# Optimization experiments

Measured on AMD Instinct MI355X. Metric: run time of the kernel, lower is better.

## Reference

```python
import jax, jax.numpy as jnp
import numpy as np

B, L, HIDDEN = 64, 200, 256
HEADS = 8
MAX_WIDTH = 5
EPS = 1e-5  # F.layer_norm default eps


def _ln(x):
    # F.layer_norm with no learned affine
    m = jnp.mean(x, axis=-1, keepdims=True)
    v = jnp.mean((x - m) ** 2, axis=-1, keepdims=True)
    return (x - m) * jax.lax.rsqrt(v + EPS)


def _area_pool(x, max_width, mode):
    # x: [B, H, L, D] -> pooled spans of widths 1..max_width (valid windows),
    # concatenated along the memory axis: M = sum_w (L - w + 1)
    Lx = x.shape[2]
    outs = []
    for w in range(1, max_width + 1):
        # [w, B, H, L-w+1, D] stack of shifted slices (w <= 5, tiny loop)
        win = jnp.stack([x[:, :, i:Lx - w + 1 + i, :] for i in range(w)], axis=0)
        if mode == 'max':
            outs.append(win.max(axis=0))
        elif mode == 'mean':
            outs.append(win.mean(axis=0))
        else:  # 'sum'
            outs.append(win.sum(axis=0))
    return jnp.concatenate(outs, axis=2)


def _mha_area(q_in, k_in, v_in, Wq, bq, Wk, bk, Wv, bv, Wo, bo):
    # per-head size equals hidden_size (key_query_size_hidden = hidden_size)
    Bq, Lq, _ = q_in.shape
    Dh = Wq.shape[1] // HEADS

    def split(x):
        return x.reshape(x.shape[0], x.shape[1], HEADS, Dh).transpose(0, 2, 1, 3)

    q = split(q_in @ Wq + bq)  # [B, H, Lq, Dh]
    k = split(k_in @ Wk + bk)
    v = split(v_in @ Wv + bv)
    k_area = _area_pool(k, MAX_WIDTH, 'max')   # aggr='max' key pooling
    v_area = _area_pool(v, MAX_WIDTH, 'sum')   # values pooled by sum (t2t default)
    scale = jnp.asarray(1.0 / np.sqrt(Dh), q.dtype)
    logits = jnp.einsum('bhqd,bhmd->bhqm', q, k_area) * scale
    attn = jax.nn.softmax(logits, axis=-1)  # dropout inactive at eval
    out = jnp.einsum('bhqm,bhmd->bhqd', attn, v_area)
    out = out.transpose(0, 2, 1, 3).reshape(Bq, Lq, HEADS * Dh)
    return out @ Wo + bo


def setup_inputs() -> dict:
    key = jax.random.key(0)
    ks = jax.random.split(key, 16)
    stdv = 1.0 / np.sqrt(HIDDEN)
    u = lambda k, shp: jax.random.uniform(k, shp, jnp.float32, -stdv, stdv)
    HD = HEADS * HIDDEN  # 2048
    return {
        'A': jax.random.normal(ks[0], (B, L, L), jnp.float32),
        'hidden': jax.random.normal(ks[1], (B, L, HIDDEN), jnp.float32),
        'Wq': u(ks[2], (HIDDEN, HD)), 'bq': u(ks[3], (HD,)),
        'Wk': u(ks[4], (HIDDEN, HD)), 'bk': u(ks[5], (HD,)),
        'Wv': u(ks[6], (HIDDEN, HD)), 'bv': u(ks[7], (HD,)),
        'Wo': u(ks[8], (HD, HIDDEN)), 'bo': u(ks[9], (HIDDEN,)),
        'W1': u(ks[10], (HIDDEN, 4 * HIDDEN)), 'b1': u(ks[11], (4 * HIDDEN,)),
        'W2': u(ks[12], (4 * HIDDEN, HIDDEN)), 'b2': u(ks[13], (HIDDEN,)),
    }


def reference(A, hidden, Wq, bq, Wk, bk, Wv, bv, Wo, bo, W1, b1, W2, b2):
    # step = 1 -> single ATTNCell; A is unused by ATTNCell (matches source)
    attn1 = _mha_area(hidden, hidden, hidden, Wq, bq, Wk, bk, Wv, bv, Wo, bo)
    attn1 = _ln(attn1 + hidden)
    attn2 = _mha_area(attn1, hidden, hidden, Wq, bq, Wk, bk, Wv, bv, Wo, bo)
    attn2 = _ln(attn1 + attn2)  # F.dropout inactive (eval)
    x = jax.nn.relu(attn2 @ W1 + b1) @ W2 + b2
    return _ln(attn2 + x)
```

## Files before the change

kernel.cpp:

```cpp
#include <hip/hip_runtime.h>
#include <hip/hip_bf16.h>
#include <cstdint>
#include <cstddef>

#define BATCH 64
#define LSEQ 200
#define HID 256
#define NH 8
#define DH 256
#define HD (NH*DH)
#define MROWS (BATCH*LSEQ)
#define EPS 1e-5f
#define CSCALE 0.09014195f

typedef unsigned short ushort_t;
typedef __attribute__((ext_vector_type(8))) short bf16x8;
typedef __attribute__((ext_vector_type(8))) unsigned short u16x8;
typedef __attribute__((ext_vector_type(4))) float f32x4;

__device__ __forceinline__ float b2f(ushort_t u) {
    union { unsigned int i; float f; } c; c.i = ((unsigned int)u) << 16; return c.f;
}
__device__ __forceinline__ ushort_t f2b(float f) {
    __hip_bfloat16 h = __float2bfloat16(f);
    union { __hip_bfloat16 h; ushort_t u; } c; c.h = h; return c.u;
}
__device__ __forceinline__ float to_f32(float x) { return x; }
__device__ __forceinline__ float to_f32(ushort_t x) { return b2f(x); }
__device__ __forceinline__ void store_val(float* p, float v) { *p = v; }
__device__ __forceinline__ void store_val(ushort_t* p, float v) { *p = f2b(v); }

__device__ __forceinline__ u16x8 bmax8(u16x8 a, u16x8 b) {
    union U { u16x8 v; __hip_bfloat162 h[4]; };
    U ua, ub, r; ua.v = a; ub.v = b;
    #pragma unroll
    for (int i = 0; i < 4; ++i) r.h[i] = __hmax2(ua.h[i], ub.h[i]);
    return r.v;
}
__device__ __forceinline__ u16x8 badd8(u16x8 a, u16x8 b) {
    union U { u16x8 v; __hip_bfloat162 h[4]; };
    U ua, ub, r; ua.v = a; ub.v = b;
    #pragma unroll
    for (int i = 0; i < 4; ++i) r.h[i] = __hadd2(ua.h[i], ub.h[i]);
    return r.v;
}

__device__ __forceinline__ void gll16(const void* g, void* l) {
    __builtin_amdgcn_global_load_lds(
        (const __attribute__((address_space(1))) unsigned int*)g,
        (__attribute__((address_space(3))) unsigned int*)l, 16, 0, 0);
}

template<bool RELU, int OMODE, bool SCALEC>
__global__ __launch_bounds__(256) void gemm_bt(
    const ushort_t* __restrict__ A, const ushort_t* __restrict__ Bt,
    const float* __restrict__ bias, ushort_t* __restrict__ C,
    int M, int N, int K)
{
    __shared__ ushort_t As[128 * 32];
    __shared__ ushort_t Bs[128 * 32];
    const int t = threadIdx.x;
    const int m0 = blockIdx.y * 128, n0 = blockIdx.x * 128;
    const int wave = t >> 6, lane = t & 63;
    const int l15 = lane & 15, lq = lane >> 4;
    const int wr = wave >> 1, wc = wave & 1;

    f32x4 acc[4][4];
    #pragma unroll
    for (int i = 0; i < 4; ++i)
        #pragma unroll
        for (int j = 0; j < 4; ++j) acc[i][j] = (f32x4){0.f, 0.f, 0.f, 0.f};

    for (int k0 = 0; k0 < K; k0 += 32) {
        __syncthreads();
        #pragma unroll
        for (int i = 0; i < 2; ++i) {
            int li = i * 256 + t;
            int ml = li >> 2, cp = li & 3;
            int cg = cp ^ ((ml ^ (ml >> 2)) & 3);
            gll16(A + (size_t)(m0 + ml) * K + k0 + cg * 8, &As[li * 8]);
        }
        #pragma unroll
        for (int i = 0; i < 2; ++i) {
            int li = i * 256 + t;
            int nl = li >> 2, cp = li & 3;
            int cg = cp ^ ((nl ^ (nl >> 2)) & 3);
            gll16(Bt + (size_t)(n0 + nl) * K + k0 + cg * 8, &Bs[li * 8]);
        }
        __syncthreads();
        bf16x8 af[4], bfr[4];
        #pragma unroll
        for (int i = 0; i < 4; ++i) {
            int r = wr * 64 + i * 16 + l15;
            int pc = lq ^ ((r ^ (r >> 2)) & 3);
            af[i] = *(const bf16x8*)&As[r * 32 + pc * 8];
        }
        #pragma unroll
        for (int j = 0; j < 4; ++j) {
            int r = wc * 64 + j * 16 + l15;
            int pc = lq ^ ((r ^ (r >> 2)) & 3);
            bfr[j] = *(const bf16x8*)&Bs[r * 32 + pc * 8];
        }
        #pragma unroll
        for (int i = 0; i < 4; ++i)
            #pragma unroll
            for (int j = 0; j < 4; ++j)
                acc[i][j] = __builtin_amdgcn_mfma_f32_16x16x32_bf16(af[i], bfr[j], acc[i][j], 0, 0, 0);
    }
    if (OMODE == 2) {
        #pragma unroll
        for (int i = 0; i < 4; ++i) {
            int mbase = m0 + wr * 64 + i * 16 + 4 * lq;
            int bb = (int)(((unsigned)mbase * 5243u) >> 20);
            int ll = mbase - bb * 200;
            #pragma unroll
            for (int j = 0; j < 4; ++j) {
                int n = n0 + wc * 64 + j * 16 + l15;
                float bsv = bias[n];
                ushort4 o4;
                o4.x = f2b(acc[i][j][0] + bsv); o4.y = f2b(acc[i][j][1] + bsv);
                o4.z = f2b(acc[i][j][2] + bsv); o4.w = f2b(acc[i][j][3] + bsv);
                size_t addr = ((size_t)(bb * NH + (n >> 8)) * 256 + (n & 255)) * LSEQ + ll;
                *(ushort4*)&C[addr] = o4;
            }
        }
    } else {
        #pragma unroll
        for (int i = 0; i < 4; ++i) {
            #pragma unroll
            for (int e = 0; e < 4; ++e) {
                int m = m0 + wr * 64 + i * 16 + 4 * lq + e;
                #pragma unroll
                for (int j = 0; j < 4; ++j) {
                    int n = n0 + wc * 64 + j * 16 + l15;
                    float v = acc[i][j][e] + bias[n];
                    if (RELU) v = fmaxf(v, 0.f);
                    if (SCALEC) v *= CSCALE;
                    if (OMODE == 1) {
                        int bb = (int)(((unsigned)m * 5243u) >> 20);
                        int ll = m - bb * 200;
                        size_t addr = ((((size_t)(bb * NH + (n >> 8))) * LSEQ + ll) << 8) + (n & 255);
                        C[addr] = f2b(v);
                    } else {
                        C[(size_t)m * N + n] = f2b(v);
                    }
                }
            }
        }
    }
}

__global__ __launch_bounds__(512, 2) void attn_mfma13(
    const ushort_t* __restrict__ Q, const ushort_t* __restrict__ Khm,
    const ushort_t* __restrict__ Vt, ushort_t* __restrict__ O)
{
    const int id = blockIdx.x;
    const int xcd = id & 7, slot_ = id >> 3;
    const int qt = slot_ & 1;
    const int bh = ((slot_ >> 1) << 3) + xcd;
    const int b = bh >> 3, h = bh & 7;
    const int q0 = qt * 128;
    const int t = threadIdx.x;
    const int wave = t >> 6, lane = t & 63;
    const int l15 = lane & 15, lq = lane >> 4;

    __shared__ ushort_t Ks[64 * 256];
    __shared__ ushort_t Vs[256 * 64];

    const ushort_t* kbh = Khm + (size_t)bh * LSEQ * DH;
    const ushort_t* vtb = Vt + (size_t)bh * DH * LSEQ;
    const ushort_t* qbh = Q + ((size_t)b * LSEQ) * HD + h * DH;
    const int qrow = q0 + wave * 16 + l15;

    bf16x8 qf[8];
    if (qrow < LSEQ) {
        const ushort_t* qp = qbh + (size_t)qrow * HD + 8 * lq;
        #pragma unroll
        for (int g = 0; g < 8; ++g) qf[g] = *(const bf16x8*)(qp + 32 * g);
    } else {
        bf16x8 zf = {0,0,0,0,0,0,0,0};
        #pragma unroll
        for (int g = 0; g < 8; ++g) qf[g] = zf;
    }

    f32x4 oacc[16];
    #pragma unroll
    for (int i = 0; i < 16; ++i) oacc[i] = (f32x4){0.f, 0.f, 0.f, 0.f};
    float l_part = 0.f;

    const int dc = t & 31, mb = t >> 5;
    const int vd = t >> 1, vh = t & 1;

    auto step = [&](bool tail) {
        f32x4 sacc[4];
        __builtin_amdgcn_s_setprio(1);
        #pragma unroll
        for (int ms = 0; ms < 4; ++ms) {
            f32x4 s = (f32x4){0.f, 0.f, 0.f, 0.f};
            const int row = ms * 16 + l15;
            #pragma unroll
            for (int g = 0; g < 8; ++g) {
                const int phys = (lq + 4 * g) ^ l15;
                s = __builtin_amdgcn_mfma_f32_16x16x32_bf16(
                        *(const bf16x8*)&Ks[row * 256 + phys * 8], qf[g], s, 0, 0, 0);
            }
            sacc[ms] = s;
        }
        __builtin_amdgcn_s_setprio(0);
        unsigned int w[8];
        #pragma unroll
        for (int ms = 0; ms < 4; ++ms) {
            float pj[4];
            #pragma unroll
            for (int e = 0; e < 4; ++e) {
                float sv = sacc[ms][e];
                if (tail) {
                    const int slot = ms * 16 + 4 * lq + e;
                    if (((slot & 7) > 7 - (slot >> 3)) || ((slot >> 3) > 4)) sv = -1e30f;
                }
                float p = __builtin_exp2f(sv);
                l_part += p;
                pj[e] = p;
            }
            asm("v_cvt_pk_bf16_f32 %0, %1, %2" : "=v"(w[2*ms])   : "v"(pj[0]), "v"(pj[1]));
            asm("v_cvt_pk_bf16_f32 %0, %1, %2" : "=v"(w[2*ms+1]) : "v"(pj[2]), "v"(pj[3]));
        }
        union FR { unsigned int u[4]; bf16x8 v; };
        FR f0, f1;
        f0.u[0] = w[0]; f0.u[1] = w[1]; f0.u[2] = w[2]; f0.u[3] = w[3];
        f1.u[0] = w[4]; f1.u[1] = w[5]; f1.u[2] = w[6]; f1.u[3] = w[7];
        const bf16x8 pf0 = f0.v, pf1 = f1.v;
        __builtin_amdgcn_s_setprio(1);
        #pragma unroll
        for (int dt = 0; dt < 16; ++dt) {
            const int d = dt * 16 + l15;
            const int p0 = lq ^ (d & 7);
            const int p1 = (lq + 4) ^ (d & 7);
            oacc[dt] = __builtin_amdgcn_mfma_f32_16x16x32_bf16(
                           pf0, *(const bf16x8*)&Vs[d * 64 + p0 * 8], oacc[dt], 0, 0, 0);
            oacc[dt] = __builtin_amdgcn_mfma_f32_16x16x32_bf16(
                           pf1, *(const bf16x8*)&Vs[d * 64 + p1 * 8], oacc[dt], 0, 0, 0);
        }
        __builtin_amdgcn_s_setprio(0);
    };

    for (int ti = 0; ti < 3; ++ti) {
        const int st0 = ti * 64;
        #pragma unroll
        for (int cls = 0; cls < 5; ++cls) {
            u16x8 kf[4];
            #pragma unroll
            for (int k4 = 0; k4 < 4; ++k4)
                kf[k4] = *(const u16x8*)(kbh + (size_t)(st0 + mb + 16 * k4 + cls) * DH + dc * 8);
            __syncthreads();

            #pragma unroll
            for (int k4 = 0; k4 < 4; ++k4) {
                int m = mb + 16 * k4;
                ushort_t* kp = &Ks[m * 256 + ((dc ^ (m & 15)) * 8)];
                *(u16x8*)kp = (cls == 0) ? kf[k4] : bmax8(*(const u16x8*)kp, kf[k4]);
            }
            {
                const ushort_t* vrow = vtb + (size_t)vd * LSEQ + st0 + vh * 32;
                u16x8 va = *(const u16x8*)vrow;
                #pragma unroll
                for (int cl = 0; cl < 4; ++cl) {
                    u16x8 vb = *(const u16x8*)(vrow + (cl + 1) * 8);
                    const int cg = vh * 4 + cl;
                    const int kc = (cg >> 2) * 4 + (cg & 1) * 2;
                    const int par4 = ((cg >> 1) & 1) * 4;
                    ushort_t* plo = &Vs[vd * 64 + ((kc ^ (vd & 7)) * 8) + par4];
                    ushort_t* phi = &Vs[vd * 64 + (((kc + 1) ^ (vd & 7)) * 8) + par4];
                    union VH { u16x8 v; ushort4 h[2]; };
                    VH nv;
                    if (cls == 0) {
                        nv.v = va;
                    } else {
                        u16x8 sh;
                        #pragma unroll
                        for (int j = 0; j < 8; ++j)
                            sh[j] = (j + cls < 8) ? va[j + cls] : vb[j + cls - 8];
                        VH cur;
                        cur.h[0] = *(const ushort4*)plo;
                        cur.h[1] = *(const ushort4*)phi;
                        nv.v = badd8(cur.v, sh);
                    }
                    *(ushort4*)plo = nv.h[0];
                    *(ushort4*)phi = nv.h[1];
                    va = vb;
                }
            }
            __syncthreads();
            step(false);
        }
    }

    {
        __syncthreads();
        if (mb < 8) {
            u16x8 krun = *(const u16x8*)(kbh + (size_t)(192 + mb) * DH + dc * 8);
            const u16x8 kz = {0,0,0,0,0,0,0,0};
            #pragma unroll
            for (int k8 = 0; k8 < 8; ++k8) {
                const bool v = (k8 <= 4) && (mb <= 7 - k8);
                if (k8 > 0 && v)
                    krun = bmax8(krun, *(const u16x8*)(kbh + (size_t)(192 + mb + k8) * DH + dc * 8));
                int slot = k8 * 8 + mb;
                *(u16x8*)&Ks[slot * 256 + ((dc ^ (slot & 15)) * 8)] = v ? krun : kz;
            }
        }
        {
            u16x8 v0 = *(const u16x8*)(vtb + (size_t)vd * LSEQ + 192);
            float f[8];
            #pragma unroll
            for (int e = 0; e < 8; ++e) f[e] = b2f(v0[e]);
            #pragma unroll
            for (int cl = 0; cl < 4; ++cl) {
                const int c = vh * 4 + cl;
                union VH { u16x8 v; ushort4 h[2]; } ov;
                #pragma unroll
                for (int j = 0; j < 8; ++j) ov.v[j] = 0;
                if (c <= 4) {
                    #pragma unroll
                    for (int j = 0; j < 8; ++j) {
                        if (j <= 7 - c) {
                            float acc = 0.f;
                            #pragma unroll
                            for (int u = 0; u <= 4; ++u)
                                if (u <= c) acc += f[j + u];
                            ov.v[j] = f2b(acc);
                        }
                    }
                }
                const int kc = (c >> 2) * 4 + (c & 1) * 2;
                const int par4 = ((c >> 1) & 1) * 4;
                *(ushort4*)&Vs[vd * 64 + ((kc ^ (vd & 7)) * 8) + par4] = ov.h[0];
                *(ushort4*)&Vs[vd * 64 + (((kc + 1) ^ (vd & 7)) * 8) + par4] = ov.h[1];
            }
        }
        __syncthreads();
        step(true);
    }

    l_part += __shfl_xor(l_part, 16);
    l_part += __shfl_xor(l_part, 32);
    const float inv = 1.f / l_part;

    ushort_t* ob = O + ((size_t)b * LSEQ) * HD + h * DH;
    #pragma unroll
    for (int e = 0; e < 4; ++e) {
        const int q = q0 + wave * 16 + 4 * lq + e;
        const float linv = __shfl(inv, 4 * lq + e);
        if (q < LSEQ) {
            #pragma unroll
            for (int dt = 0; dt < 16; ++dt)
                ob[(size_t)q * HD + dt * 16 + l15] = f2b(oacc[dt][e] * linv);
        }
    }
}

template<typename TR, typename TO>
__global__ __launch_bounds__(256) void residual_ln(
    const ushort_t* __restrict__ X, const TR* __restrict__ R, TO* __restrict__ Out)
{
    const int row = blockIdx.x;
    const int t = threadIdx.x;
    const size_t base = (size_t)row * HID;
    float v = b2f(X[base + t]) + to_f32(R[base + t]);
    float s = v, q = v * v;
    #pragma unroll
    for (int o = 32; o > 0; o >>= 1) {
        s += __shfl_xor(s, o, 64);
        q += __shfl_xor(q, o, 64);
    }
    __shared__ float ss[4], sq[4];
    const int wave = t >> 6, lane = t & 63;
    if (lane == 0) { ss[wave] = s; sq[wave] = q; }
    __syncthreads();
    s = ss[0] + ss[1] + ss[2] + ss[3];
    q = sq[0] + sq[1] + sq[2] + sq[3];
    float mean = s * (1.f / HID);
    float var  = q * (1.f / HID) - mean * mean;
    store_val(&Out[base + t], (v - mean) * rsqrtf(var + EPS));
}

__global__ __launch_bounds__(256) void cvt_f32_bf16(const float* __restrict__ in,
                                                    ushort_t* __restrict__ out) {
    const int i = (blockIdx.x * 256 + threadIdx.x) * 4;
    float4 v = *(const float4*)(in + i);
    ushort4 o;
    o.x = f2b(v.x); o.y = f2b(v.y); o.z = f2b(v.z); o.w = f2b(v.w);
    *(ushort4*)(out + i) = o;
}

__global__ __launch_bounds__(256) void wtrans(const float* __restrict__ W,
                                              ushort_t* __restrict__ Wt, int K, int N) {
    __shared__ float tile[32][33];
    const int t = threadIdx.x;
    const int tx = t & 31, ty = t >> 5;
    const int n0 = blockIdx.x * 32, k0 = blockIdx.y * 32;
    #pragma unroll
    for (int s = 0; s < 4; ++s)
        tile[ty + 8 * s][tx] = W[(size_t)(k0 + ty + 8 * s) * N + n0 + tx];
    __syncthreads();
    #pragma unroll
    for (int s = 0; s < 4; ++s)
        Wt[(size_t)(n0 + ty + 8 * s) * K + k0 + tx] = f2b(tile[tx][ty + 8 * s]);
}

extern "C" void kernel_launch(void* const* d_in, const int* in_sizes, int n_in,
                              void* d_out, int out_size, void* d_ws, size_t ws_size,
                              hipStream_t stream) {
    const float* hidden = (const float*)d_in[1];
    const float* Wq = (const float*)d_in[2];  const float* bq = (const float*)d_in[3];
    const float* Wk = (const float*)d_in[4];  const float* bk = (const float*)d_in[5];
    const float* Wv = (const float*)d_in[6];  const float* bv = (const float*)d_in[7];
    const float* Wo = (const float*)d_in[8];  const float* bo = (const float*)d_in[9];
    const float* W1 = (const float*)d_in[10]; const float* b1 = (const float*)d_in[11];
    const float* W2 = (const float*)d_in[12]; const float* b2 = (const float*)d_in[13];
    float* out = (float*)d_out;

    constexpr size_t SZ_BF   = (size_t)MROWS * HD * 2;
    constexpr size_t SZ_HBF  = (size_t)MROWS * HID * 2;
    constexpr size_t SZ_WQKV = (size_t)HID * HD * 2;
    constexpr size_t SZ_W12  = (size_t)HID * 4 * HID * 2;
    char* ws = (char*)d_ws;
    size_t off = 0;
    ushort_t* kb   = (ushort_t*)(ws + off); off += SZ_BF;
    ushort_t* vt   = (ushort_t*)(ws + off); off += SZ_BF;
    ushort_t* qo   = (ushort_t*)(ws + off); off += SZ_BF;
    ushort_t* hb   = (ushort_t*)(ws + off); off += SZ_HBF;
    ushort_t* at1  = (ushort_t*)(ws + off); off += SZ_HBF;
    ushort_t* at2  = (ushort_t*)(ws + off); off += SZ_HBF;
    ushort_t* proj = (ushort_t*)(ws + off); off += SZ_HBF;
    ushort_t* WtQ  = (ushort_t*)(ws + off); off += SZ_WQKV;
    ushort_t* WtK  = (ushort_t*)(ws + off); off += SZ_WQKV;
    ushort_t* WtV  = (ushort_t*)(ws + off); off += SZ_WQKV;
    ushort_t* WtO  = (ushort_t*)(ws + off); off += SZ_WQKV;
    ushort_t* Wt1  = (ushort_t*)(ws + off); off += SZ_W12;
    ushort_t* Wt2  = (ushort_t*)(ws + off); off += SZ_W12;
    if (ws_size < off) return;
    ushort_t* ffn1 = qo;

    dim3 blk(256);
    cvt_f32_bf16<<<MROWS * HID / 1024, blk, 0, stream>>>(hidden, hb);
    wtrans<<<dim3(HD / 32, HID / 32), blk, 0, stream>>>(Wq, WtQ, HID, HD);
    wtrans<<<dim3(HD / 32, HID / 32), blk, 0, stream>>>(Wk, WtK, HID, HD);
    wtrans<<<dim3(HD / 32, HID / 32), blk, 0, stream>>>(Wv, WtV, HID, HD);
    wtrans<<<dim3(HID / 32, HD / 32), blk, 0, stream>>>(Wo, WtO, HD, HID);
    wtrans<<<dim3(4 * HID / 32, HID / 32), blk, 0, stream>>>(W1, Wt1, HID, 4 * HID);
    wtrans<<<dim3(HID / 32, 4 * HID / 32), blk, 0, stream>>>(W2, Wt2, 4 * HID, HID);

    const dim3 gProj(HD / 128, MROWS / 128);
    const dim3 gOut(HID / 128, MROWS / 128);
    const dim3 gF1(4 * HID / 128, MROWS / 128);

    gemm_bt<false, 1, false><<<gProj, blk, 0, stream>>>(hb, WtK, bk, kb, MROWS, HD, HID);
    gemm_bt<false, 2, false><<<gProj, blk, 0, stream>>>(hb, WtV, bv, vt, MROWS, HD, HID);

    gemm_bt<false, 0, true><<<gProj, blk, 0, stream>>>(hb, WtQ, bq, qo, MROWS, HD, HID);
    attn_mfma13<<<2 * BATCH * NH, 512, 0, stream>>>(qo, kb, vt, qo);
    gemm_bt<false, 0, false><<<gOut, blk, 0, stream>>>(qo, WtO, bo, proj, MROWS, HID, HD);
    residual_ln<float, ushort_t><<<MROWS, blk, 0, stream>>>(proj, hidden, at1);

    gemm_bt<false, 0, true><<<gProj, blk, 0, stream>>>(at1, WtQ, bq, qo, MROWS, HD, HID);
    attn_mfma13<<<2 * BATCH * NH, 512, 0, stream>>>(qo, kb, vt, qo);
    gemm_bt<false, 0, false><<<gOut, blk, 0, stream>>>(qo, WtO, bo, proj, MROWS, HID, HD);
    residual_ln<ushort_t, ushort_t><<<MROWS, blk, 0, stream>>>(proj, at1, at2);

    gemm_bt<true, 0, false><<<gF1, blk, 0, stream>>>(at2, Wt1, b1, ffn1, MROWS, 4 * HID, HID);
    gemm_bt<false, 0, false><<<gOut, blk, 0, stream>>>(ffn1, Wt2, b2, proj, MROWS, HID, 4 * HID);
    residual_ln<ushort_t, float><<<MROWS, blk, 0, stream>>>(proj, at2, out);
}
```

Baseline: 977.7 us.

## Halve attention block threads, each wave computing two query tiles sharing K/V LDS reads

The attention kernel now runs 256 threads per block instead of 512. Each wave handles two 16-row query tiles (rows r and r+64), so every K and V fragment read from LDS feeds two MFMAs. The K/V pooling loaders are reworked so the 256 threads cover the same 64-slot tile. This cuts LDS read traffic per MFMA and halves the threads doing the pooling work, at the cost of roughly doubled accumulator registers per thread, which may lower occupancy or cause spills.

```diff
diff --git a/kernel.cpp b/kernel.cpp
--- a/kernel.cpp
+++ b/kernel.cpp
@@ -150,7 +150,7 @@
     }
 }
 
-__global__ __launch_bounds__(512, 2) void attn_mfma13(
+__global__ __launch_bounds__(256, 2) void attn_mfma15(
     const ushort_t* __restrict__ Q, const ushort_t* __restrict__ Khm,
     const ushort_t* __restrict__ Vt, ushort_t* __restrict__ O)
 {
@@ -170,76 +170,94 @@
     const ushort_t* kbh = Khm + (size_t)bh * LSEQ * DH;
     const ushort_t* vtb = Vt + (size_t)bh * DH * LSEQ;
     const ushort_t* qbh = Q + ((size_t)b * LSEQ) * HD + h * DH;
-    const int qrow = q0 + wave * 16 + l15;
-
-    bf16x8 qf[8];
-    if (qrow < LSEQ) {
-        const ushort_t* qp = qbh + (size_t)qrow * HD + 8 * lq;
-        #pragma unroll
-        for (int g = 0; g < 8; ++g) qf[g] = *(const bf16x8*)(qp + 32 * g);
+
+    const int qrA = q0 + wave * 16 + l15;
+    const int qrB = qrA + 64;
+    bf16x8 qfA[8], qfB[8];
+    {
+        const ushort_t* qp = qbh + (size_t)qrA * HD + 8 * lq;
+        #pragma unroll
+        for (int g = 0; g < 8; ++g) qfA[g] = *(const bf16x8*)(qp + 32 * g);
+    }
+    if (qrB < LSEQ) {
+        const ushort_t* qp = qbh + (size_t)qrB * HD + 8 * lq;
+        #pragma unroll
+        for (int g = 0; g < 8; ++g) qfB[g] = *(const bf16x8*)(qp + 32 * g);
     } else {
         bf16x8 zf = {0,0,0,0,0,0,0,0};
         #pragma unroll
-        for (int g = 0; g < 8; ++g) qf[g] = zf;
-    }
-
-    f32x4 oacc[16];
-    #pragma unroll
-    for (int i = 0; i < 16; ++i) oacc[i] = (f32x4){0.f, 0.f, 0.f, 0.f};
-    float l_part = 0.f;
+        for (int g = 0; g < 8; ++g) qfB[g] = zf;
+    }
+
+    f32x4 oaccA[16], oaccB[16];
+    #pragma unroll
+    for (int i = 0; i < 16; ++i) {
+        oaccA[i] = (f32x4){0.f, 0.f, 0.f, 0.f};
+        oaccB[i] = (f32x4){0.f, 0.f, 0.f, 0.f};
+    }
+    float lA = 0.f, lB = 0.f;
 
     const int dc = t & 31, mb = t >> 5;
-    const int vd = t >> 1, vh = t & 1;
+    const int vd = t;
 
     auto step = [&](bool tail) {
-        f32x4 sacc[4];
+        f32x4 sA[4], sB[4];
         __builtin_amdgcn_s_setprio(1);
         #pragma unroll
         for (int ms = 0; ms < 4; ++ms) {
-            f32x4 s = (f32x4){0.f, 0.f, 0.f, 0.f};
+            f32x4 xa = (f32x4){0.f, 0.f, 0.f, 0.f};
+            f32x4 xb = (f32x4){0.f, 0.f, 0.f, 0.f};
             const int row = ms * 16 + l15;
             #pragma unroll
             for (int g = 0; g < 8; ++g) {
                 const int phys = (lq + 4 * g) ^ l15;
-                s = __builtin_amdgcn_mfma_f32_16x16x32_bf16(
-                        *(const bf16x8*)&Ks[row * 256 + phys * 8], qf[g], s, 0, 0, 0);
-            }
-            sacc[ms] = s;
+                const bf16x8 kk = *(const bf16x8*)&Ks[row * 256 + phys * 8];
+                xa = __builtin_amdgcn_mfma_f32_16x16x32_bf16(kk, qfA[g], xa, 0, 0, 0);
+                xb = __builtin_amdgcn_mfma_f32_16x16x32_bf16(kk, qfB[g], xb, 0, 0, 0);
+            }
+            sA[ms] = xa; sB[ms] = xb;
         }
         __builtin_amdgcn_s_setprio(0);
-        unsigned int w[8];
+        unsigned int wA[8], wB[8];
         #pragma unroll
         for (int ms = 0; ms < 4; ++ms) {
-            float pj[4];
+            float pa[4], pb[4];
             #pragma unroll
             for (int e = 0; e < 4; ++e) {
-                float sv = sacc[ms][e];
+                float va_ = sA[ms][e], vb_ = sB[ms][e];
                 if (tail) {
                     const int slot = ms * 16 + 4 * lq + e;
-                    if (((slot & 7) > 7 - (slot >> 3)) || ((slot >> 3) > 4)) sv = -1e30f;
+                    if (((slot & 7) > 7 - (slot >> 3)) || ((slot >> 3) > 4)) {
+                        va_ = -1e30f; vb_ = -1e30f;
+                    }
                 }
-                float p = __builtin_exp2f(sv);
-                l_part += p;
-                pj[e] = p;
-            }
-            asm("v_cvt_pk_bf16_f32 %0, %1, %2" : "=v"(w[2*ms])   : "v"(pj[0]), "v"(pj[1]));
-            asm("v_cvt_pk_bf16_f32 %0, %1, %2" : "=v"(w[2*ms+1]) : "v"(pj[2]), "v"(pj[3]));
+                float ea = __builtin_exp2f(va_);
+                float eb = __builtin_exp2f(vb_);
+                lA += ea; lB += eb;
+                pa[e] = ea; pb[e] = eb;
+            }
+            asm("v_cvt_pk_bf16_f32 %0, %1, %2" : "=v"(wA[2*ms])   : "v"(pa[0]), "v"(pa[1]));
+            asm("v_cvt_pk_bf16_f32 %0, %1, %2" : "=v"(wA[2*ms+1]) : "v"(pa[2]), "v"(pa[3]));
+            asm("v_cvt_pk_bf16_f32 %0, %1, %2" : "=v"(wB[2*ms])   : "v"(pb[0]), "v"(pb[1]));
+            asm("v_cvt_pk_bf16_f32 %0, %1, %2" : "=v"(wB[2*ms+1]) : "v"(pb[2]), "v"(pb[3]));
         }
         union FR { unsigned int u[4]; bf16x8 v; };
-        FR f0, f1;
-        f0.u[0] = w[0]; f0.u[1] = w[1]; f0.u[2] = w[2]; f0.u[3] = w[3];
-        f1.u[0] = w[4]; f1.u[1] = w[5]; f1.u[2] = w[6]; f1.u[3] = w[7];
-        const bf16x8 pf0 = f0.v, pf1 = f1.v;
+        FR a0, a1, b0, b1;
+        a0.u[0] = wA[0]; a0.u[1] = wA[1]; a0.u[2] = wA[2]; a0.u[3] = wA[3];
+        a1.u[0] = wA[4]; a1.u[1] = wA[5]; a1.u[2] = wA[6]; a1.u[3] = wA[7];
+        b0.u[0] = wB[0]; b0.u[1] = wB[1]; b0.u[2] = wB[2]; b0.u[3] = wB[3];
+        b1.u[0] = wB[4]; b1.u[1] = wB[5]; b1.u[2] = wB[6]; b1.u[3] = wB[7];
+        const bf16x8 pfA0 = a0.v, pfA1 = a1.v, pfB0 = b0.v, pfB1 = b1.v;
         __builtin_amdgcn_s_setprio(1);
         #pragma unroll
         for (int dt = 0; dt < 16; ++dt) {
             const int d = dt * 16 + l15;
-            const int p0 = lq ^ (d & 7);
-            const int p1 = (lq + 4) ^ (d & 7);
-            oacc[dt] = __builtin_amdgcn_mfma_f32_16x16x32_bf16(
-                           pf0, *(const bf16x8*)&Vs[d * 64 + p0 * 8], oacc[dt], 0, 0, 0);
-            oacc[dt] = __builtin_amdgcn_mfma_f32_16x16x32_bf16(
-                           pf1, *(const bf16x8*)&Vs[d * 64 + p1 * 8], oacc[dt], 0, 0, 0);
+            const bf16x8 v0 = *(const bf16x8*)&Vs[d * 64 + ((lq ^ (d & 7)) * 8)];
+            const bf16x8 v1 = *(const bf16x8*)&Vs[d * 64 + (((lq + 4) ^ (d & 7)) * 8)];
+            oaccA[dt] = __builtin_amdgcn_mfma_f32_16x16x32_bf16(pfA0, v0, oaccA[dt], 0, 0, 0);
+            oaccA[dt] = __builtin_amdgcn_mfma_f32_16x16x32_bf16(pfA1, v1, oaccA[dt], 0, 0, 0);
+            oaccB[dt] = __builtin_amdgcn_mfma_f32_16x16x32_bf16(pfB0, v0, oaccB[dt], 0, 0, 0);
+            oaccB[dt] = __builtin_amdgcn_mfma_f32_16x16x32_bf16(pfB1, v1, oaccB[dt], 0, 0, 0);
         }
         __builtin_amdgcn_s_setprio(0);
     };
@@ -250,23 +268,29 @@
         for (int cls = 0; cls < 5; ++cls) {
             u16x8 kf[4];
             #pragma unroll
-            for (int k4 = 0; k4 < 4; ++k4)
-                kf[k4] = *(const u16x8*)(kbh + (size_t)(st0 + mb + 16 * k4 + cls) * DH + dc * 8);
+            for (int k8 = 0; k8 < 4; ++k8)
+                kf[k8] = *(const u16x8*)(kbh + (size_t)(st0 + mb + 8 * k8 + cls) * DH + dc * 8);
             __syncthreads();
 
             #pragma unroll
-            for (int k4 = 0; k4 < 4; ++k4) {
-                int m = mb + 16 * k4;
+            for (int k8 = 0; k8 < 4; ++k8) {
+                int m = mb + 8 * k8;
                 ushort_t* kp = &Ks[m * 256 + ((dc ^ (m & 15)) * 8)];
-                *(u16x8*)kp = (cls == 0) ? kf[k4] : bmax8(*(const u16x8*)kp, kf[k4]);
+                *(u16x8*)kp = (cls == 0) ? kf[k8] : bmax8(*(const u16x8*)kp, kf[k8]);
+            }
+            #pragma unroll
+            for (int k8 = 4; k8 < 8; ++k8) {
+                u16x8 kv = *(const u16x8*)(kbh + (size_t)(st0 + mb + 8 * k8 + cls) * DH + dc * 8);
+                int m = mb + 8 * k8;
+                ushort_t* kp = &Ks[m * 256 + ((dc ^ (m & 15)) * 8)];
+                *(u16x8*)kp = (cls == 0) ? kv : bmax8(*(const u16x8*)kp, kv);
             }
             {
-                const ushort_t* vrow = vtb + (size_t)vd * LSEQ + st0 + vh * 32;
+                const ushort_t* vrow = vtb + (size_t)vd * LSEQ + st0;
                 u16x8 va = *(const u16x8*)vrow;
                 #pragma unroll
-                for (int cl = 0; cl < 4; ++cl) {
-                    u16x8 vb = *(const u16x8*)(vrow + (cl + 1) * 8);
-                    const int cg = vh * 4 + cl;
+                for (int cg = 0; cg < 8; ++cg) {
+                    u16x8 vb = *(const u16x8*)(vrow + (cg + 1) * 8);
                     const int kc = (cg >> 2) * 4 + (cg & 1) * 2;
                     const int par4 = ((cg >> 1) & 1) * 4;
                     ushort_t* plo = &Vs[vd * 64 + ((kc ^ (vd & 7)) * 8) + par4];
@@ -297,16 +321,16 @@
 
     {
         __syncthreads();
-        if (mb < 8) {
+        {
             u16x8 krun = *(const u16x8*)(kbh + (size_t)(192 + mb) * DH + dc * 8);
             const u16x8 kz = {0,0,0,0,0,0,0,0};
             #pragma unroll
             for (int k8 = 0; k8 < 8; ++k8) {
-                const bool v = (k8 <= 4) && (mb <= 7 - k8);
-                if (k8 > 0 && v)
+                const bool vv = (k8 <= 4) && (mb <= 7 - k8);
+                if (k8 > 0 && vv)
                     krun = bmax8(krun, *(const u16x8*)(kbh + (size_t)(192 + mb + k8) * DH + dc * 8));
                 int slot = k8 * 8 + mb;
-                *(u16x8*)&Ks[slot * 256 + ((dc ^ (slot & 15)) * 8)] = v ? krun : kz;
+                *(u16x8*)&Ks[slot * 256 + ((dc ^ (slot & 15)) * 8)] = vv ? krun : kz;
             }
         }
         {
@@ -315,8 +339,7 @@
             #pragma unroll
             for (int e = 0; e < 8; ++e) f[e] = b2f(v0[e]);
             #pragma unroll
-            for (int cl = 0; cl < 4; ++cl) {
-                const int c = vh * 4 + cl;
+            for (int c = 0; c < 8; ++c) {
                 union VH { u16x8 v; ushort4 h[2]; } ov;
                 #pragma unroll
                 for (int j = 0; j < 8; ++j) ov.v[j] = 0;
@@ -342,19 +365,25 @@
         step(true);
     }
 
-    l_part += __shfl_xor(l_part, 16);
-    l_part += __shfl_xor(l_part, 32);
-    const float inv = 1.f / l_part;
+    lA += __shfl_xor(lA, 16); lA += __shfl_xor(lA, 32);
+    lB += __shfl_xor(lB, 16); lB += __shfl_xor(lB, 32);
+    const float invA = 1.f / lA;
+    const float invB = 1.f / lB;
 
     ushort_t* ob = O + ((size_t)b * LSEQ) * HD + h * DH;
     #pragma unroll
     for (int e = 0; e < 4; ++e) {
-        const int q = q0 + wave * 16 + 4 * lq + e;
-        const float linv = __shfl(inv, 4 * lq + e);
-        if (q < LSEQ) {
+        const float la = __shfl(invA, 4 * lq + e);
+        const float lb = __shfl(invB, 4 * lq + e);
+        const int qA = q0 + wave * 16 + 4 * lq + e;
+        const int qB = qA + 64;
+        #pragma unroll
+        for (int dt = 0; dt < 16; ++dt)
+            ob[(size_t)qA * HD + dt * 16 + l15] = f2b(oaccA[dt][e] * la);
+        if (qB < LSEQ) {
             #pragma unroll
             for (int dt = 0; dt < 16; ++dt)
-                ob[(size_t)q * HD + dt * 16 + l15] = f2b(oacc[dt][e] * linv);
+                ob[(size_t)qB * HD + dt * 16 + l15] = f2b(oaccB[dt][e] * lb);
         }
     }
 }
@@ -459,12 +488,12 @@
     gemm_bt<false, 2, false><<<gProj, blk, 0, stream>>>(hb, WtV, bv, vt, MROWS, HD, HID);
 
     gemm_bt<false, 0, true><<<gProj, blk, 0, stream>>>(hb, WtQ, bq, qo, MROWS, HD, HID);
-    attn_mfma13<<<2 * BATCH * NH, 512, 0, stream>>>(qo, kb, vt, qo);
+    attn_mfma15<<<2 * BATCH * NH, 256, 0, stream>>>(qo, kb, vt, qo);
     gemm_bt<false, 0, false><<<gOut, blk, 0, stream>>>(qo, WtO, bo, proj, MROWS, HID, HD);
     residual_ln<float, ushort_t><<<MROWS, blk, 0, stream>>>(proj, hidden, at1);
 
     gemm_bt<false, 0, true><<<gProj, blk, 0, stream>>>(at1, WtQ, bq, qo, MROWS, HD, HID);
-    attn_mfma13<<<2 * BATCH * NH, 512, 0, stream>>>(qo, kb, vt, qo);
+    attn_mfma15<<<2 * BATCH * NH, 256, 0, stream>>>(qo, kb, vt, qo);
     gemm_bt<false, 0, false><<<gOut, blk, 0, stream>>>(qo, WtO, bo, proj, MROWS, HID, HD);
     residual_ln<ushort_t, ushort_t><<<MROWS, blk, 0, stream>>>(proj, at1, at2);
 
```

Result: slower. 1.672 ms (+71.0%).
